# Kernel optimization log

Measured on AMD Instinct MI355X. Metric: run time of the kernel, lower is better.

Reference implementation:

```python
import jax, jax.numpy as jnp
import numpy as np
import math

N, Tp1, V = 256, 33, 10000
D_FEAT, H, W_DIM = 1280, 512, 256
NULL_IDX = 0


def setup_inputs() -> dict:
    key = jax.random.key(0)
    ks = jax.random.split(key, 10)
    feats = jax.random.normal(ks[0], (N, D_FEAT, 4, 4), dtype=jnp.float32)
    captions = jax.random.randint(ks[1], (N, Tp1), 0, V)
    W_proj = jax.random.normal(ks[2], (D_FEAT, H), dtype=jnp.float32) / math.sqrt(D_FEAT)
    b_proj = jnp.zeros((H,), dtype=jnp.float32)
    W_embed = jax.random.normal(ks[3], (V, W_DIM), dtype=jnp.float32) / math.sqrt(V)
    Wx = jax.random.normal(ks[4], (W_DIM, 4 * H), dtype=jnp.float32) / math.sqrt(W_DIM)
    Wh = jax.random.normal(ks[5], (H, 4 * H), dtype=jnp.float32) / math.sqrt(H)
    Wattn = jax.random.normal(ks[6], (H, 4 * H), dtype=jnp.float32) / math.sqrt(H)
    b = jnp.zeros((4 * H,), dtype=jnp.float32)
    W_vocab = jax.random.normal(ks[7], (H, V), dtype=jnp.float32) / math.sqrt(H)
    b_vocab = jnp.zeros((V,), dtype=jnp.float32)
    return {"feats": feats, "captions": captions, "W_proj": W_proj, "b_proj": b_proj,
            "W_embed": W_embed, "Wx": Wx, "Wh": Wh, "Wattn": Wattn, "b": b,
            "W_vocab": W_vocab, "b_vocab": b_vocab}


def _attention_lstm(x, A_flat, h0, Wx, Wh, Wattn, b):
    # x: (N,T,W), A_flat: (N,H,16), h0: (N,H)
    Hh = h0.shape[1]
    scale = 1.0 / math.sqrt(Hh)

    def step(carry, x_t):
        h, c = carry
        # scaled dot-product attention over the 16 spatial positions
        scores = jnp.einsum('nh,nhp->np', h, A_flat) * scale       # (N,16)
        w = jax.nn.softmax(scores, axis=1)
        attn = jnp.einsum('nhp,np->nh', A_flat, w)                 # (N,H)
        a = x_t @ Wx + h @ Wh + b + attn @ Wattn                   # (N,4H)
        i = jax.nn.sigmoid(a[:, 0:Hh])
        f = jax.nn.sigmoid(a[:, Hh:2 * Hh])
        o = jax.nn.sigmoid(a[:, 2 * Hh:3 * Hh])
        g = jnp.tanh(a[:, 3 * Hh:4 * Hh])
        c_next = f * c + i * g
        h_next = o * jnp.tanh(c_next)
        return (h_next, c_next), h_next

    (_, _), hs = jax.lax.scan(step, (h0, h0), jnp.swapaxes(x, 0, 1))
    return jnp.swapaxes(hs, 0, 1)  # (N,T,H)


def reference(feats, captions, W_proj, b_proj, W_embed, Wx, Wh, Wattn, b, W_vocab, b_vocab):
    cap_in = captions[:, :-1]   # (N,T)
    cap_out = captions[:, 1:]   # (N,T)
    # project CNN features per spatial location: (N,Dfeat,4,4) -> (N,H,4,4)
    A = jnp.einsum('ncij,ch->nhij', feats, W_proj) + b_proj[None, :, None, None]
    h0 = A.mean(axis=(2, 3))                     # (N,H); c0 = h0
    A_flat = A.reshape(A.shape[0], A.shape[1], 16)
    x = W_embed[cap_in]                           # (N,T,W)
    h = _attention_lstm(x, A_flat, h0, Wx, Wh, Wattn, b)
    scores = jnp.einsum('nth,hv->ntv', h, W_vocab) + b_vocab   # (N,T,V)
    # temporal softmax loss, sum over tokens (ignoring NULL), averaged over N
    logp = jax.nn.log_softmax(scores, axis=-1)
    nll = -jnp.take_along_axis(logp, cap_out[..., None], axis=-1)[..., 0]  # (N,T)
    mask = (cap_out != NULL_IDX).astype(scores.dtype)
    loss = jnp.sum(nll * mask) / scores.shape[0]
    return loss
```

## Files before the change

kernel.cpp:

```cpp
#include <hip/hip_runtime.h>
#include <hip/hip_bf16.h>

#define NB   256
#define NT   32
#define NV   10000
#define NVP  10240
#define NDF  1280
#define NH   512
#define VT_N 40

typedef short bf16x8 __attribute__((ext_vector_type(8)));
typedef float f32x4  __attribute__((ext_vector_type(4)));
typedef unsigned short u16;

__device__ __forceinline__ float b2f(u16 u) {
    union { unsigned i; float f; } v; v.i = ((unsigned)u) << 16; return v.f;
}
__device__ __forceinline__ u16 f2b(float f) {
    union { float f; unsigned i; } v; v.f = f;
    unsigned r = v.i + 0x7FFF + ((v.i >> 16) & 1);
    return (u16)(r >> 16);
}

__device__ __forceinline__ void gload16(const u16* g, u16* l) {
    __builtin_amdgcn_global_load_lds(
        (const __attribute__((address_space(1))) void*)g,
        (__attribute__((address_space(3))) void*)l, 16, 0, 0);
}

static const size_t B_C     = 0;
static const size_t B_SCP   = B_C     + (size_t)256*512*4;
static const size_t B_PMAX  = B_SCP   + (size_t)2*32*256*16*4;
static const size_t B_PSUM  = B_PMAX  + (size_t)8192*VT_N*4;
static const size_t B_TGT   = B_PSUM  + (size_t)8192*VT_N*4;
static const size_t B_LOSS  = B_TGT   + (size_t)8192*4;
static const size_t B_AB    = B_LOSS  + 16;
static const size_t B_XPB   = B_AB    + (size_t)256*16*512*2;
static const size_t B_HALLB = B_XPB   + (size_t)32*256*2048*2;
static const size_t B_WVT   = B_HALLB + (size_t)32*256*512*2;
static const size_t B_WXT   = B_WVT   + (size_t)10240*512*2;
static const size_t B_WHAT  = B_WXT   + (size_t)2048*256*2;
static const size_t B_HB0   = B_WHAT  + (size_t)2048*1024*2;
static const size_t B_HB1   = B_HB0   + (size_t)256*512*2;
static const size_t B_PREAW = B_HB1   + (size_t)256*512*2;

__global__ __launch_bounds__(256) void tconv_kernel(
    const float* __restrict__ src, u16* __restrict__ dst,
    int K, int N, int Npad, int ldK, int koff)
{
    __shared__ u16 tile[64][65];
    const int k0 = blockIdx.y * 64, n0 = blockIdx.x * 64, tid = threadIdx.x;
#pragma unroll
    for (int i = 0; i < 16; i++) {
        int idx = tid + i * 256;
        int kk = idx >> 6, nn = idx & 63;
        int n = n0 + nn;
        float v = (n < N) ? src[(size_t)(k0 + kk) * N + n] : 0.f;
        tile[kk][nn] = f2b(v);
    }
    __syncthreads();
#pragma unroll
    for (int i = 0; i < 16; i++) {
        int idx = tid + i * 256;
        int nn = idx >> 6, kk = idx & 63;
        int n = n0 + nn;
        if (n < Npad) dst[(size_t)n * ldK + koff + k0 + kk] = tile[kk][nn];
    }
}

__global__ __launch_bounds__(256) void ftrans_kernel(
    const float* __restrict__ feats, u16* __restrict__ fT)
{
    const int cch = blockIdx.x, n = blockIdx.y, tid = threadIdx.x;
    __shared__ u16 lt[64][17];
    const int c0 = cch * 64;
    const int c = tid >> 2, p4 = (tid & 3) * 4;
    float4 v = *(const float4*)(feats + (size_t)n * 20480 + (size_t)(c0 + c) * 16 + p4);
    lt[c][p4] = f2b(v.x); lt[c][p4 + 1] = f2b(v.y);
    lt[c][p4 + 2] = f2b(v.z); lt[c][p4 + 3] = f2b(v.w);
    __syncthreads();
    const int p = tid >> 4, cg = tid & 15;
    ushort4 o;
    o.x = lt[cg * 4 + 0][p]; o.y = lt[cg * 4 + 1][p];
    o.z = lt[cg * 4 + 2][p]; o.w = lt[cg * 4 + 3][p];
    *(ushort4*)(fT + (size_t)(n * 16 + p) * 1280 + c0 + cg * 4) = o;
}

__global__ __launch_bounds__(256) void proj_gemm_kernel(
    const u16* __restrict__ fT, const u16* __restrict__ WpT,
    const float* __restrict__ bp, u16* __restrict__ Ab)
{
    const int rt = blockIdx.x;
    const int tid = threadIdx.x, w = tid >> 6, lane = tid & 63;
    const int r0 = rt * 64;
    const int lm = lane & 15, lkq = lane >> 4, lk = lkq * 8;
    const int nbase = w * 128;

    f32x4 acc[4][8];
#pragma unroll
    for (int mt = 0; mt < 4; mt++)
#pragma unroll
        for (int nt = 0; nt < 8; nt++) acc[mt][nt] = (f32x4){0.f, 0.f, 0.f, 0.f};

    for (int kc = 0; kc < 1280; kc += 32) {
        bf16x8 af[4];
#pragma unroll
        for (int mt = 0; mt < 4; mt++)
            af[mt] = *(const bf16x8*)(fT + (size_t)(r0 + mt * 16 + lm) * 1280 + kc + lk);
#pragma unroll
        for (int nt = 0; nt < 8; nt++) {
            bf16x8 bfg = *(const bf16x8*)(WpT + (size_t)(nbase + nt * 16 + lm) * 1280 + kc + lk);
#pragma unroll
            for (int mt = 0; mt < 4; mt++)
                acc[mt][nt] = __builtin_amdgcn_mfma_f32_16x16x32_bf16(af[mt], bfg, acc[mt][nt], 0, 0, 0);
        }
    }
    float bbv[8];
#pragma unroll
    for (int nt = 0; nt < 8; nt++) bbv[nt] = bp[nbase + nt * 16 + lm];
#pragma unroll
    for (int mt = 0; mt < 4; mt++)
#pragma unroll
        for (int nt = 0; nt < 8; nt++)
#pragma unroll
            for (int r = 0; r < 4; r++) {
                int row = r0 + mt * 16 + lkq * 4 + r;
                int col = nbase + nt * 16 + lm;
                Ab[(size_t)row * 512 + col] = f2b(acc[mt][nt][r] + bbv[nt]);
            }
}

__global__ __launch_bounds__(256) void projmean_kernel(
    const u16* __restrict__ Ab, float* __restrict__ c0, u16* __restrict__ hb0)
{
    const int n = blockIdx.x, tid = threadIdx.x;
    const int col0 = tid, col1 = tid + 256;
    float s0 = 0.f, s1 = 0.f;
#pragma unroll
    for (int p = 0; p < 16; p++) {
        const u16* ap = Ab + ((size_t)n * 16 + p) * 512;
        s0 += b2f(ap[col0]);
        s1 += b2f(ap[col1]);
    }
    s0 *= 0.0625f; s1 *= 0.0625f;
    c0[n * 512 + col0] = s0;  c0[n * 512 + col1] = s1;
    hb0[(size_t)n * 512 + col0] = f2b(s0);
    hb0[(size_t)n * 512 + col1] = f2b(s1);
}

__global__ __launch_bounds__(256) void xp_mfma_kernel(
    const int* __restrict__ caps, const float* __restrict__ We,
    const u16* __restrict__ Wxt, const float* __restrict__ bb,
    u16* __restrict__ xpb)
{
    const int ct = blockIdx.x, rt = blockIdx.y;
    const int tid = threadIdx.x, w = tid >> 6, lane = tid & 63;
    const int r0 = rt * 64;
    const int lm = lane & 15, lkq = lane >> 4, lk = lkq * 8;
    const int nbase = ct * 512 + w * 128;

    int capm[4];
#pragma unroll
    for (int mt = 0; mt < 4; mt++) {
        int row = r0 + mt * 16 + lm;
        capm[mt] = caps[(row >> 5) * 33 + (row & 31)];
    }
    f32x4 acc[4][8];
#pragma unroll
    for (int mt = 0; mt < 4; mt++)
#pragma unroll
        for (int nt = 0; nt < 8; nt++) acc[mt][nt] = (f32x4){0.f, 0.f, 0.f, 0.f};

    for (int kc = 0; kc < 256; kc += 32) {
        bf16x8 af[4];
#pragma unroll
        for (int mt = 0; mt < 4; mt++) {
            const float* ap = We + (size_t)capm[mt] * 256 + kc + lk;
            float4 f0 = *(const float4*)ap;
            float4 f1 = *(const float4*)(ap + 4);
            bf16x8 t;
            t[0] = (short)f2b(f0.x); t[1] = (short)f2b(f0.y);
            t[2] = (short)f2b(f0.z); t[3] = (short)f2b(f0.w);
            t[4] = (short)f2b(f1.x); t[5] = (short)f2b(f1.y);
            t[6] = (short)f2b(f1.z); t[7] = (short)f2b(f1.w);
            af[mt] = t;
        }
#pragma unroll
        for (int nt = 0; nt < 8; nt++) {
            bf16x8 bfg = *(const bf16x8*)(Wxt + (size_t)(nbase + nt * 16 + lm) * 256 + kc + lk);
#pragma unroll
            for (int mt = 0; mt < 4; mt++)
                acc[mt][nt] = __builtin_amdgcn_mfma_f32_16x16x32_bf16(af[mt], bfg, acc[mt][nt], 0, 0, 0);
        }
    }
    float bbv[8];
#pragma unroll
    for (int nt = 0; nt < 8; nt++) bbv[nt] = bb[nbase + nt * 16 + lm];
#pragma unroll
    for (int mt = 0; mt < 4; mt++)
#pragma unroll
        for (int nt = 0; nt < 8; nt++)
#pragma unroll
            for (int r = 0; r < 4; r++) {
                int row = r0 + mt * 16 + lkq * 4 + r;
                int col = nbase + nt * 16 + lm;
                float v = acc[mt][nt][r] + bbv[nt];
                xpb[((size_t)(row & 31) * 256 + (row >> 5)) * 2048 + col] = f2b(v);
            }
}

__global__ __launch_bounds__(256) void preaw_mfma_kernel(
    const u16* __restrict__ Ab, const u16* __restrict__ what,
    u16* __restrict__ preaw)
{
    const int ct = blockIdx.x, rt = blockIdx.y;
    const int tid = threadIdx.x, w = tid >> 6, lane = tid & 63;
    const int r0 = rt * 64;
    const int lm = lane & 15, lkq = lane >> 4, lk = lkq * 8;
    const int nbase = ct * 512 + w * 128;

    f32x4 acc[4][8];
#pragma unroll
    for (int mt = 0; mt < 4; mt++)
#pragma unroll
        for (int nt = 0; nt < 8; nt++) acc[mt][nt] = (f32x4){0.f, 0.f, 0.f, 0.f};

    for (int kc = 0; kc < 512; kc += 32) {
        bf16x8 af[4];
#pragma unroll
        for (int mt = 0; mt < 4; mt++) {
            int row = r0 + mt * 16 + lm;
            af[mt] = *(const bf16x8*)(Ab + ((size_t)(row & 255) * 16 + (row >> 8)) * 512 + kc + lk);
        }
#pragma unroll
        for (int nt = 0; nt < 8; nt++) {
            bf16x8 bfg = *(const bf16x8*)(what + (size_t)(nbase + nt * 16 + lm) * 1024 + 512 + kc + lk);
#pragma unroll
            for (int mt = 0; mt < 4; mt++)
                acc[mt][nt] = __builtin_amdgcn_mfma_f32_16x16x32_bf16(af[mt], bfg, acc[mt][nt], 0, 0, 0);
        }
    }
#pragma unroll
    for (int mt = 0; mt < 4; mt++)
#pragma unroll
        for (int nt = 0; nt < 8; nt++)
#pragma unroll
            for (int r = 0; r < 4; r++) {
                int row = r0 + mt * 16 + lkq * 4 + r;
                int col = nbase + nt * 16 + lm;
                preaw[(size_t)row * 2048 + col] = f2b(acc[mt][nt][r]);
            }
}

__global__ __launch_bounds__(64) void score_init_kernel(
    const u16* __restrict__ hb0, const u16* __restrict__ Ab,
    float* __restrict__ scp)
{
    const int n = blockIdx.x, lane = threadIdx.x;
    const u16* hp = hb0 + (size_t)n * 512 + lane * 8;
    ushort4 h0 = *(const ushort4*)hp, h1 = *(const ushort4*)(hp + 4);
    float hv0 = b2f(h0.x), hv1 = b2f(h0.y), hv2 = b2f(h0.z), hv3 = b2f(h0.w);
    float hv4 = b2f(h1.x), hv5 = b2f(h1.y), hv6 = b2f(h1.z), hv7 = b2f(h1.w);
    float mine = 0.f;
#pragma unroll
    for (int p = 0; p < 16; p++) {
        const u16* ap = Ab + (size_t)n * 8192 + p * 512 + lane * 8;
        ushort4 a0 = *(const ushort4*)ap, a1 = *(const ushort4*)(ap + 4);
        float s = hv0*b2f(a0.x) + hv1*b2f(a0.y) + hv2*b2f(a0.z) + hv3*b2f(a0.w)
                + hv4*b2f(a1.x) + hv5*b2f(a1.y) + hv6*b2f(a1.z) + hv7*b2f(a1.w);
#pragma unroll
        for (int mask = 1; mask <= 32; mask <<= 1) s += __shfl_xor(s, mask, 64);
        if (lane == p) mine = s;
    }
    if (lane < 16) scp[n * 16 + lane] = mine;
    for (int i = lane; i < 31 * 16; i += 64)
        scp[(1 + (i >> 4)) * 4096 + n * 16 + (i & 15)] = 0.f;
}

__global__ __launch_bounds__(256) void gates_fused_kernel(
    const u16* __restrict__ hb_in, const float* __restrict__ scp_in,
    const u16* __restrict__ what, const u16* __restrict__ preaw,
    const u16* __restrict__ xpt, const u16* __restrict__ Ab,
    float* __restrict__ c, u16* __restrict__ hb_out,
    u16* __restrict__ hallbt, float* __restrict__ scp_out)
{
    const int rt = blockIdx.x, cg = blockIdx.y;
    const int tid = threadIdx.x, ty = tid >> 6, lane = tid & 63;
    const int lm = lane & 15, lkq = lane >> 4, lk = lkq * 8;
    const int r0 = rt * 16, hc0 = cg * 16;

    __shared__ u16 hs[16 * 520];
    __shared__ float sred[16][17];
    __shared__ float wts[16][17];
    __shared__ float gred[3][64][4];
    __shared__ u16 hnew[16][16];

#pragma unroll
    for (int i = 0; i < 8; i++) {
        int fid = tid + i * 256;
        int r = fid >> 7, c4 = fid & 127;
        *(ushort4*)&hs[r * 520 + c4 * 4] =
            *(const ushort4*)(hb_in + (size_t)(r0 + r) * 512 + c4 * 4);
    }
    {
        const int r = tid >> 4, p = tid & 15;
        float s = 0.f;
#pragma unroll
        for (int g = 0; g < 32; g++) s += scp_in[g * 4096 + (r0 + r) * 16 + p];
        sred[r][p] = s * 0.04419417382415922f;
    }
    __syncthreads();
    {
        const int r = tid >> 4, p = tid & 15;
        float m = -1e30f;
#pragma unroll
        for (int q = 0; q < 16; q++) m = fmaxf(m, sred[r][q]);
        float su = 0.f;
#pragma unroll
        for (int q = 0; q < 16; q++) su += __expf(sred[r][q] - m);
        wts[r][p] = __expf(sred[r][p] - m) / su;
    }
    __syncthreads();

    f32x4 acc = (f32x4){0.f, 0.f, 0.f, 0.f};
    const u16* brow = what + (size_t)(ty * 512 + hc0 + lm) * 1024 + lk;
    const u16* arow = &hs[lm * 520 + lk];
    for (int kc = 0; kc < 512; kc += 32) {
        bf16x8 af = *(const bf16x8*)(arow + kc);
        bf16x8 bfg = *(const bf16x8*)(brow + kc);
        acc = __builtin_amdgcn_mfma_f32_16x16x32_bf16(af, bfg, acc, 0, 0, 0);
    }
    float val[4];
#pragma unroll
    for (int r = 0; r < 4; r++) {
        const int rl = lkq * 4 + r, n = r0 + rl;
        const int col = ty * 512 + hc0 + lm;
        float s = acc[r] + b2f(xpt[(size_t)n * 2048 + col]);
#pragma unroll
        for (int p = 0; p < 16; p++)
            s += wts[rl][p] * b2f(preaw[((size_t)p * 256 + n) * 2048 + col]);
        val[r] = s;
    }
    if (ty > 0) {
#pragma unroll
        for (int r = 0; r < 4; r++) gred[ty - 1][lane][r] = val[r];
    }
    __syncthreads();
    if (ty == 0) {
#pragma unroll
        for (int r = 0; r < 4; r++) {
            const int rl = lkq * 4 + r, n = r0 + rl;
            const int hcol = hc0 + lm;
            float ai  = val[r];
            float af_ = gred[0][lane][r];
            float ao  = gred[1][lane][r];
            float ag  = gred[2][lane][r];
            float ig = 1.f / (1.f + __expf(-ai));
            float fg = 1.f / (1.f + __expf(-af_));
            float og = 1.f / (1.f + __expf(-ao));
            float gv = tanhf(ag);
            const int idx = n * 512 + hcol;
            float cn = fg * c[idx] + ig * gv;
            float hn = og * tanhf(cn);
            c[idx] = cn;
            u16 hbv = f2b(hn);
            hb_out[idx] = hbv;
            hallbt[idx] = hbv;
            hnew[rl][lm] = hbv;
        }
    }
    __syncthreads();
    {
        const int r = tid >> 4, p = tid & 15, n = r0 + r;
        const u16* ap = Ab + (size_t)n * 8192 + p * 512 + hc0;
        float s = 0.f;
#pragma unroll
        for (int j = 0; j < 16; j++) s += b2f(hnew[r][j]) * b2f(ap[j]);
        scp_out[cg * 4096 + n * 16 + p] = s;
    }
}

__global__ __launch_bounds__(512) void vocab_mfma_kernel(
    const u16* __restrict__ hallb, const u16* __restrict__ Wvt,
    const float* __restrict__ bv, const int* __restrict__ caps,
    float* __restrict__ pmax, float* __restrict__ psum, float* __restrict__ tgt)
{
    const int ct = blockIdx.x, rt = blockIdx.y;
    const int tid = threadIdx.x, w = tid >> 6, lane = tid & 63;
    const int wr = w >> 2, wc = w & 3;
    const int r0 = rt * 128, c0 = ct * 256;
    const int lm = lane & 15, lkq = lane >> 4, lk = lkq * 8;

    __shared__ u16 As[128 * 32];
    __shared__ u16 Bs[256 * 32];
    __shared__ int tvs[128];
    __shared__ float cm[128][4], cs[128][4];

    if (tid < 128) {
        int row = r0 + tid;
        tvs[tid] = caps[(row & 255) * 33 + (row >> 8) + 1];
    }

    f32x4 acc[4][4];
#pragma unroll
    for (int mt = 0; mt < 4; mt++)
#pragma unroll
        for (int nt = 0; nt < 4; nt++) acc[mt][nt] = (f32x4){0.f, 0.f, 0.f, 0.f};

    const int fa  = w * 64 + lane;
    const u16* gA  = hallb + (size_t)(r0 + (fa >> 2)) * 512 + (fa & 3) * 8;
    const int fb0 = w * 64 + lane;
    const int fb1 = fb0 + 512;
    const u16* gB0 = Wvt + (size_t)(c0 + (fb0 >> 2)) * 512 + (fb0 & 3) * 8;
    const u16* gB1 = Wvt + (size_t)(c0 + (fb1 >> 2)) * 512 + (fb1 & 3) * 8;
    u16* lA  = &As[w * 512];
    u16* lB0 = &Bs[w * 512];
    u16* lB1 = &Bs[(w + 8) * 512];

    for (int kc = 0; kc < 512; kc += 32) {
        gload16(gA  + kc, lA);
        gload16(gB0 + kc, lB0);
        gload16(gB1 + kc, lB1);
        __syncthreads();
        bf16x8 af[4], bfr[4];
#pragma unroll
        for (int mt = 0; mt < 4; mt++)
            af[mt] = *(const bf16x8*)&As[(wr * 64 + mt * 16 + lm) * 32 + lk];
#pragma unroll
        for (int nt = 0; nt < 4; nt++)
            bfr[nt] = *(const bf16x8*)&Bs[(wc * 64 + nt * 16 + lm) * 32 + lk];
#pragma unroll
        for (int nt = 0; nt < 4; nt++)
#pragma unroll
            for (int mt = 0; mt < 4; mt++)
                acc[mt][nt] = __builtin_amdgcn_mfma_f32_16x16x32_bf16(af[mt], bfr[nt], acc[mt][nt], 0, 0, 0);
        __syncthreads();
    }

    float bvv[4]; bool vld[4];
#pragma unroll
    for (int nt = 0; nt < 4; nt++) {
        int col = c0 + wc * 64 + nt * 16 + lm;
        vld[nt] = (col < NV);
        bvv[nt] = vld[nt] ? bv[col] : 0.f;
    }
#pragma unroll
    for (int mt = 0; mt < 4; mt++)
#pragma unroll
        for (int r = 0; r < 4; r++) {
            int rloc = wr * 64 + mt * 16 + lkq * 4 + r;
            int row = r0 + rloc;
            int tv = tvs[rloc];
            float vals[4]; float m = -1e30f;
#pragma unroll
            for (int nt = 0; nt < 4; nt++) {
                int col = c0 + wc * 64 + nt * 16 + lm;
                float v = vld[nt] ? (acc[mt][nt][r] + bvv[nt]) : -1e30f;
                vals[nt] = v;
                m = fmaxf(m, v);
                if (col == tv) tgt[row] = v;
            }
#pragma unroll
            for (int mask = 1; mask <= 8; mask <<= 1) m = fmaxf(m, __shfl_xor(m, mask, 64));
            float s = 0.f;
#pragma unroll
            for (int nt = 0; nt < 4; nt++) s += __expf(vals[nt] - m);
#pragma unroll
            for (int mask = 1; mask <= 8; mask <<= 1) s += __shfl_xor(s, mask, 64);
            if (lm == 0) { cm[rloc][wc] = m; cs[rloc][wc] = s; }
        }
    __syncthreads();
    if (tid < 128) {
        float M = -1e30f;
#pragma unroll
        for (int q = 0; q < 4; q++) M = fmaxf(M, cm[tid][q]);
        float S = 0.f;
#pragma unroll
        for (int q = 0; q < 4; q++) S += cs[tid][q] * __expf(cm[tid][q] - M);
        int row = r0 + tid;
        pmax[row * VT_N + ct] = M;
        psum[row * VT_N + ct] = S;
    }
}

__global__ __launch_bounds__(256) void loss_reduce_kernel(
    const float* __restrict__ pmax, const float* __restrict__ psum,
    const float* __restrict__ tgt, const int* __restrict__ caps,
    float* __restrict__ loss)
{
    const int row = blockIdx.x * 256 + threadIdx.x;
    float nll = 0.f;
    const int t = row >> 8, n = row & 255;
    const int tv = caps[n * 33 + t + 1];
    if (tv != 0) {
        float M = -1e30f;
#pragma unroll
        for (int vt = 0; vt < VT_N; vt++) M = fmaxf(M, pmax[row * VT_N + vt]);
        float S = 0.f;
#pragma unroll
        for (int vt = 0; vt < VT_N; vt++) S += psum[row * VT_N + vt] * __expf(pmax[row * VT_N + vt] - M);
        nll = logf(S) + M - tgt[row];
    }
#pragma unroll
    for (int off = 32; off; off >>= 1) nll += __shfl_down(nll, off, 64);
    __shared__ float r4[4];
    if ((threadIdx.x & 63) == 0) r4[threadIdx.x >> 6] = nll;
    __syncthreads();
    if (threadIdx.x == 0)
        atomicAdd(loss, (r4[0] + r4[1] + r4[2] + r4[3]) * (1.f / 256.f));
}

__global__ void finalize_kernel(const float* __restrict__ loss, float* __restrict__ out)
{
    if (threadIdx.x == 0 && blockIdx.x == 0) out[0] = loss[0];
}

extern "C" void kernel_launch(void* const* d_in, const int* in_sizes, int n_in,
                              void* d_out, int out_size, void* d_ws, size_t ws_size,
                              hipStream_t stream) {
    const float* feats = (const float*)d_in[0];
    const int*   caps  = (const int*)d_in[1];
    const float* Wp    = (const float*)d_in[2];
    const float* bp    = (const float*)d_in[3];
    const float* We    = (const float*)d_in[4];
    const float* Wx    = (const float*)d_in[5];
    const float* Wh    = (const float*)d_in[6];
    const float* Wattn = (const float*)d_in[7];
    const float* bb    = (const float*)d_in[8];
    const float* Wv    = (const float*)d_in[9];
    const float* bv    = (const float*)d_in[10];

    char* ws = (char*)d_ws;
    float* c     = (float*)(ws + B_C);
    float* scp0  = (float*)(ws + B_SCP);
    float* scp1  = scp0 + (size_t)32 * 4096;
    float* pmax  = (float*)(ws + B_PMAX);
    float* psum  = (float*)(ws + B_PSUM);
    float* tgt   = (float*)(ws + B_TGT);
    float* loss  = (float*)(ws + B_LOSS);
    u16*   Ab    = (u16*)(ws + B_AB);
    u16*   xpb   = (u16*)(ws + B_XPB);
    u16*   hallb = (u16*)(ws + B_HALLB);
    u16*   wvt   = (u16*)(ws + B_WVT);
    u16*   wxt   = (u16*)(ws + B_WXT);
    u16*   what  = (u16*)(ws + B_WHAT);
    u16*   hb[2] = { (u16*)(ws + B_HB0), (u16*)(ws + B_HB1) };
    u16*   preaw = (u16*)(ws + B_PREAW);
    u16*   fT    = wvt;
    u16*   WpT   = xpb;

    hipMemsetAsync(loss, 0, sizeof(float), stream);

    ftrans_kernel<<<dim3(20, 256), 256, 0, stream>>>(feats, fT);
    tconv_kernel<<<dim3(8, 20), 256, 0, stream>>>(Wp, WpT, 1280, 512, 512, 1280, 0);
    proj_gemm_kernel<<<64, 256, 0, stream>>>(fT, WpT, bp, Ab);
    projmean_kernel<<<256, 256, 0, stream>>>(Ab, c, hb[0]);

    tconv_kernel<<<dim3(160, 8), 256, 0, stream>>>(Wv, wvt, 512, NV, NVP, 512, 0);
    tconv_kernel<<<dim3(32, 4),  256, 0, stream>>>(Wx, wxt, 256, 2048, 2048, 256, 0);
    tconv_kernel<<<dim3(32, 8),  256, 0, stream>>>(Wh, what, 512, 2048, 2048, 1024, 0);
    tconv_kernel<<<dim3(32, 8),  256, 0, stream>>>(Wattn, what, 512, 2048, 2048, 1024, 512);
    xp_mfma_kernel<<<dim3(4, 128), 256, 0, stream>>>(caps, We, wxt, bb, xpb);
    preaw_mfma_kernel<<<dim3(4, 64), 256, 0, stream>>>(Ab, what, preaw);
    score_init_kernel<<<256, 64, 0, stream>>>(hb[0], Ab, scp0);

    for (int t = 0; t < NT; t++) {
        const int in = t & 1;
        gates_fused_kernel<<<dim3(16, 32), 256, 0, stream>>>(
            hb[in], in ? scp1 : scp0, what, preaw,
            xpb + (size_t)t * 524288, Ab, c,
            hb[1 - in], hallb + (size_t)t * 131072,
            in ? scp0 : scp1);
    }

    vocab_mfma_kernel<<<dim3(VT_N, 64), 512, 0, stream>>>(
        hallb, wvt, bv, caps, pmax, psum, tgt);
    loss_reduce_kernel<<<32, 256, 0, stream>>>(pmax, psum, tgt, caps, loss);
    finalize_kernel<<<1, 64, 0, stream>>>(loss, (float*)d_out);
}
```

Measured before the change: 898.2 us.

## Double-buffer vocab GEMM LDS tiles and XOR-swizzle to avoid bank conflicts

The vocab projection GEMM now uses two LDS buffers so the next K-chunk's global-to-LDS loads are issued before computing on the current chunk, with an explicit vmcnt wait and barriers. The 16-byte K groups are XOR-swizzled by row, both when storing to LDS and when reading MFMA fragments, to cut LDS bank conflicts. This targets exposed global load latency and LDS read stalls in the vocab kernel. It doubles the LDS footprint and depends on the hand-written vmcnt(3) count matching the number of outstanding loads.

```diff
diff --git a/kernel.cpp b/kernel.cpp
--- a/kernel.cpp
+++ b/kernel.cpp
@@ -389,10 +389,11 @@
     const int tid = threadIdx.x, w = tid >> 6, lane = tid & 63;
     const int wr = w >> 2, wc = w & 3;
     const int r0 = rt * 128, c0 = ct * 256;
-    const int lm = lane & 15, lkq = lane >> 4, lk = lkq * 8;
-
-    __shared__ u16 As[128 * 32];
-    __shared__ u16 Bs[256 * 32];
+    const int lm = lane & 15, lkq = lane >> 4;
+    const int swz = lkq ^ ((lm >> 1) & 3);
+
+    __shared__ u16 As[2][512 * 8];
+    __shared__ u16 Bs[2][1024 * 8];
     __shared__ int tvs[128];
     __shared__ float cm[128][4], cs[128][4];
 
@@ -407,35 +408,48 @@
 #pragma unroll
         for (int nt = 0; nt < 4; nt++) acc[mt][nt] = (f32x4){0.f, 0.f, 0.f, 0.f};
 
-    const int fa  = w * 64 + lane;
-    const u16* gA  = hallb + (size_t)(r0 + (fa >> 2)) * 512 + (fa & 3) * 8;
-    const int fb0 = w * 64 + lane;
-    const int fb1 = fb0 + 512;
-    const u16* gB0 = Wvt + (size_t)(c0 + (fb0 >> 2)) * 512 + (fb0 & 3) * 8;
-    const u16* gB1 = Wvt + (size_t)(c0 + (fb1 >> 2)) * 512 + (fb1 & 3) * 8;
-    u16* lA  = &As[w * 512];
-    u16* lB0 = &Bs[w * 512];
-    u16* lB1 = &Bs[(w + 8) * 512];
-
-    for (int kc = 0; kc < 512; kc += 32) {
-        gload16(gA  + kc, lA);
-        gload16(gB0 + kc, lB0);
-        gload16(gB1 + kc, lB1);
-        __syncthreads();
+    const int sA = w * 64 + lane;
+    const int rA = sA >> 2, kA = (sA & 3) ^ ((rA >> 1) & 3);
+    const u16* gA = hallb + (size_t)(r0 + rA) * 512 + kA * 8;
+    const int sB0 = w * 64 + lane, sB1 = sB0 + 512;
+    const int cB0 = sB0 >> 2, kB0 = (sB0 & 3) ^ ((cB0 >> 1) & 3);
+    const int cB1 = sB1 >> 2, kB1 = (sB1 & 3) ^ ((cB1 >> 1) & 3);
+    const u16* gB0 = Wvt + (size_t)(c0 + cB0) * 512 + kB0 * 8;
+    const u16* gB1 = Wvt + (size_t)(c0 + cB1) * 512 + kB1 * 8;
+
+    auto stage = [&](int buf, int kc) {
+        gload16(gA + kc, &As[buf][w * 512]);
+        gload16(gB0 + kc, &Bs[buf][w * 512]);
+        gload16(gB1 + kc, &Bs[buf][(w + 8) * 512]);
+    };
+    auto compute = [&](int buf) {
         bf16x8 af[4], bfr[4];
 #pragma unroll
         for (int mt = 0; mt < 4; mt++)
-            af[mt] = *(const bf16x8*)&As[(wr * 64 + mt * 16 + lm) * 32 + lk];
+            af[mt] = *(const bf16x8*)&As[buf][((wr * 64 + mt * 16 + lm) * 4 + swz) * 8];
 #pragma unroll
         for (int nt = 0; nt < 4; nt++)
-            bfr[nt] = *(const bf16x8*)&Bs[(wc * 64 + nt * 16 + lm) * 32 + lk];
+            bfr[nt] = *(const bf16x8*)&Bs[buf][((wc * 64 + nt * 16 + lm) * 4 + swz) * 8];
 #pragma unroll
         for (int nt = 0; nt < 4; nt++)
 #pragma unroll
             for (int mt = 0; mt < 4; mt++)
                 acc[mt][nt] = __builtin_amdgcn_mfma_f32_16x16x32_bf16(af[mt], bfr[nt], acc[mt][nt], 0, 0, 0);
-        __syncthreads();
-    }
+    };
+
+    stage(0, 0);
+#pragma unroll 1
+    for (int t = 0; t < 15; ++t) {
+        const int cur = t & 1;
+        stage(cur ^ 1, (t + 1) * 32);
+        asm volatile("s_waitcnt vmcnt(3)" ::: "memory");
+        __builtin_amdgcn_s_barrier();
+        compute(cur);
+        __builtin_amdgcn_s_barrier();
+    }
+    asm volatile("s_waitcnt vmcnt(0)" ::: "memory");
+    __builtin_amdgcn_s_barrier();
+    compute(1);
 
     float bvv[4]; bool vld[4];
 #pragma unroll
```

New measurement: 883.5 us. About the same (-1.6%).
